# Kernel tuning notes

Hardware: AMD Instinct MI355X
Metric: run time of the kernel (lower is better)

## Reference

```python
import jax, jax.numpy as jnp
import numpy as np
from jax import lax

K = 3; PAD = 1; STR = 1; DIL = 1; DG = 16; MRM = 10.0


def _conv3(x, w, b):
    y = lax.conv_general_dilated(x, w, (1, 1), ((PAD, PAD), (PAD, PAD)),
                                 dimension_numbers=('NCHW', 'OIHW', 'NCHW'))
    return y + b[None, :, None, None]


def _leaky(x):
    return jnp.where(x >= 0, x, 0.1 * x)


def _bilinear_gather(img, py, px):
    # img: [B, dg, cg, H, W]; py, px: [B, dg, KK, H, W] sampling coords
    B, dg, cg, H, W = img.shape
    KK = py.shape[2]
    y0f = jnp.floor(py); x0f = jnp.floor(px)
    wy = py - y0f; wx = px - x0f          # bilinear fractions (grad flows via py/px)
    y0 = y0f.astype(jnp.int32); x0 = x0f.astype(jnp.int32)
    y1 = y0 + 1; x1 = x0 + 1
    imgf = img.reshape(B * dg, cg, H * W)

    def gather(yi, xi):
        valid = ((yi >= 0) & (yi < H) & (xi >= 0) & (xi < W)).astype(img.dtype)
        idx = jnp.clip(yi, 0, H - 1) * W + jnp.clip(xi, 0, W - 1)
        idxf = idx.reshape(B * dg, KK * H * W)
        v = jax.vmap(lambda im, ix: im[:, ix])(imgf, idxf)  # [B*dg, cg, KK*H*W]
        v = v.reshape(B, dg, cg, KK, H, W)
        return v * valid[:, :, None]  # zero padding outside image

    w00 = ((1 - wy) * (1 - wx))[:, :, None]
    w01 = ((1 - wy) * wx)[:, :, None]
    w10 = (wy * (1 - wx))[:, :, None]
    w11 = (wy * wx)[:, :, None]
    return (gather(y0, x0) * w00 + gather(y0, x1) * w01 +
            gather(y1, x0) * w10 + gather(y1, x1) * w11)


def reference(x, extra_feat, flow, w1, b1, w2, b2, w3, b3, weight):
    B, C, H, W = x.shape
    KK = K * K
    cg = C // DG
    P = DG * KK
    # offset/mask generating convnet
    h = _leaky(_conv3(extra_feat, w1, b1))
    h = _leaky(_conv3(h, w2, b2))
    o = _conv3(h, w3, b3)                       # [B, 3*P, H, W]
    o1, o2, m = jnp.split(o, 3, axis=1)
    off = MRM * jnp.tanh(jnp.concatenate([o1, o2], axis=1))  # [B, 2P, H, W]
    flow_yx = flow[:, ::-1]                      # flip(1): (x,y)->(y,x)
    off = off + jnp.tile(flow_yx, (1, P, 1, 1))
    off = off.reshape(B, DG, KK, 2, H, W)        # pair p=(g,k): channel 2p=y, 2p+1=x
    off_y = off[:, :, :, 0]
    off_x = off[:, :, :, 1]
    mask = jax.nn.sigmoid(m).reshape(B, DG, KK, H, W)

    ki = jnp.arange(KK)
    ky = (ki // K).astype(x.dtype) * DIL - PAD   # kernel row offsets
    kx = (ki % K).astype(x.dtype) * DIL - PAD
    base_h = jnp.arange(H, dtype=x.dtype) * STR
    base_w = jnp.arange(W, dtype=x.dtype) * STR
    py = base_h[None, None, None, :, None] + ky[None, None, :, None, None] + off_y
    px = base_w[None, None, None, None, :] + kx[None, None, :, None, None] + off_x

    img = x.reshape(B, DG, cg, H, W)
    val = _bilinear_gather(img, py, px) * mask[:, :, None]  # [B,dg,cg,KK,H,W]
    wk = weight.reshape(weight.shape[0], DG, cg, KK)
    # modulated deformable conv accumulate (bias=None in original forward)
    return jnp.einsum('bgckhw,ogck->bohw', val, wk)


def setup_inputs() -> dict:
    key = jax.random.key(0)
    ks = jax.random.split(key, 10)
    B, C, H, W = 2, 64, 128, 128
    OFFC = 3 * K * K * DG  # 432
    return {
        'x': jax.random.normal(ks[0], (B, C, H, W), jnp.float32),
        'extra_feat': jax.random.normal(ks[1], (B, 2 * C, H, W), jnp.float32),
        'flow': jax.random.normal(ks[2], (B, 2, H, W), jnp.float32),
        'w1': jax.random.normal(ks[3], (C, 2 * C, 3, 3), jnp.float32) * 0.05,
        'b1': jnp.zeros((C,), jnp.float32),
        'w2': jax.random.normal(ks[4], (C, C, 3, 3), jnp.float32) * 0.05,
        'b2': jnp.zeros((C,), jnp.float32),
        'w3': jax.random.normal(ks[5], (OFFC, C, 3, 3), jnp.float32) * 0.01,
        'b3': jnp.zeros((OFFC,), jnp.float32),
        'weight': jax.random.normal(ks[6], (C, C, 3, 3), jnp.float32) * 0.05,
    }
```

## Files before the change

### kernel.cpp

```cpp
#include <hip/hip_runtime.h>
#include <math.h>

constexpr int B_   = 2;
constexpr int C_   = 64;
constexpr int H_   = 128;
constexpr int W_   = 128;
constexpr int HW_  = H_ * W_;
constexpr int DG_  = 16;
constexpr int KK_  = 9;
constexpr int CG_  = 4;
constexpr int OFFC_ = 3 * KK_ * DG_;
constexpr int R_   = C_ * KK_;
constexpr int WP_  = 130;
constexpr int HWP_ = WP_ * WP_;

typedef _Float16 half8 __attribute__((ext_vector_type(8)));
typedef _Float16 half4 __attribute__((ext_vector_type(4)));
typedef float floatx4 __attribute__((ext_vector_type(4)));

__device__ __forceinline__ void gl_lds16(const _Float16* g, _Float16* l)
{
    __builtin_amdgcn_global_load_lds(
        (const __attribute__((address_space(1))) void*)g,
        (__attribute__((address_space(3))) void*)l, 16, 0, 0);
}

__device__ __forceinline__ int afrag_src(int c)
{
    const int cmf = c >> 6, cq = (c >> 4) & 3, cl = c & 15;
    return (cmf * 16 + cl) * 32 + cq * 8;
}

constexpr int SR0 = 288, SR1 = 432, SR2 = 1404, SR3 = 1548;
constexpr int SR4 = 1676, SR5 = 1804, SR6 = 1837;

__global__ __launch_bounds__(256) void setup_k(
    const float* __restrict__ x,  const float* __restrict__ ef,
    const float* __restrict__ w1, const float* __restrict__ w2,
    const float* __restrict__ w3, const float* __restrict__ wk,
    _Float16* __restrict__ w1A, _Float16* __restrict__ w2A,
    _Float16* __restrict__ w3A, _Float16* __restrict__ wkA,
    _Float16* __restrict__ ef_p, _Float16* __restrict__ xg,
    _Float16* __restrict__ h1p,  _Float16* __restrict__ h2p)
{
    const int bid = blockIdx.x;
    const int tid = threadIdx.x;

    if (bid < SR0) {
        constexpr int OC = 64, CH = 4;
        const int j = bid * 256 + tid;
        if (j >= 9 * CH * OC * 32) return;
        const int slab = j / (OC * 32);
        const int rem  = j - slab * (OC * 32);
        const int oc   = rem >> 5;
        const int jj   = rem & 31;
        const int t    = slab / CH;
        const int h    = slab - t * CH;
        const int ic   = h * 32 + jj;
        w1A[j] = (_Float16)w1[(size_t)oc * (128 * 9) + ic * 9 + t];
    } else if (bid < SR1) {
        constexpr int OC = 64, CH = 2;
        const int j = (bid - SR0) * 256 + tid;
        if (j >= 9 * CH * OC * 32) return;
        const int slab = j / (OC * 32);
        const int rem  = j - slab * (OC * 32);
        const int oc   = rem >> 5;
        const int jj   = rem & 31;
        const int t    = slab / CH;
        const int h    = slab - t * CH;
        const int ic   = h * 32 + jj;
        w2A[j] = (_Float16)w2[(size_t)oc * (64 * 9) + ic * 9 + t];
    } else if (bid < SR2) {
        constexpr int OC = OFFC_, CH = 2;
        const int j = (bid - SR1) * 256 + tid;
        if (j >= 9 * CH * OC * 32) return;
        const int slab = j / (OC * 32);
        const int rem  = j - slab * (OC * 32);
        const int oc   = rem >> 5;
        const int jj   = rem & 31;
        const int t    = slab / CH;
        const int h    = slab - t * CH;
        const int ic   = h * 32 + jj;
        w3A[j] = (_Float16)w3[(size_t)oc * (64 * 9) + ic * 9 + t];
    } else if (bid < SR3) {
        const int j = (bid - SR2) * 256 + tid;
        if (j >= 18 * 64 * 32) return;
        const int s   = j >> 11;
        const int rem = j & 2047;
        const int oc  = rem >> 5;
        const int jj  = rem & 31;
        const int k   = s >> 1;
        const int gc  = (s & 1) * 32 + jj;
        wkA[j] = (_Float16)wk[(size_t)oc * R_ + gc * 9 + k];
    } else if (bid < SR4) {
        const int lb  = bid - SR3;
        const int b   = lb >> 6;
        const int pix = (lb & 63) * 256 + tid;
        const int yp  = pix >> 7;
        const int xp  = pix & (W_ - 1);
        const float* ib = ef + (size_t)b * 128 * HW_ + pix;
#pragma unroll
        for (int c0 = 0; c0 < 128; c0 += 8) {
            half8 v;
#pragma unroll
            for (int j = 0; j < 8; ++j)
                v[j] = (_Float16)ib[(size_t)(c0 + j) * HW_];
            const int slab = c0 >> 5;
            *(half8*)&ef_p[((size_t)(slab * B_ + b) * HWP_
                            + (size_t)(yp + 1) * WP_ + (xp + 1)) * 32 + (c0 & 31)] = v;
        }
    } else if (bid < SR5) {
        const int lb  = bid - SR4;
        const int b   = lb >> 6;
        const int pix = (lb & 63) * 256 + tid;
        const float* ib = x + (size_t)b * C_ * HW_ + pix;
#pragma unroll
        for (int g = 0; g < DG_; ++g) {
            half4 v;
#pragma unroll
            for (int c = 0; c < 4; ++c)
                v[c] = (_Float16)ib[(size_t)(g * 4 + c) * HW_];
            *(half4*)&xg[((size_t)(b * DG_ + g) * HW_ + pix) * 4] = v;
        }
    } else {
        const int idx = (bid - SR5) * 256 + tid;
        if (idx >= 16 * 516) return;
        const int plane = idx / 516;
        const int p     = idx - plane * 516;
        int yp, xp;
        if (p < 130)      { yp = 0;            xp = p; }
        else if (p < 260) { yp = 129;          xp = p - 130; }
        else if (p < 388) { yp = 1 + (p - 260); xp = 0; }
        else              { yp = 1 + (p - 388); xp = 129; }
        _Float16* base;
        if (plane < 8)       base = ef_p + (size_t)plane * HWP_ * 32;
        else if (plane < 12) base = h1p + (size_t)(plane - 8) * HWP_ * 32;
        else                 base = h2p + (size_t)(plane - 12) * HWP_ * 32;
        _Float16* dst = base + ((size_t)yp * WP_ + xp) * 32;
        const half8 z = (half8){0, 0, 0, 0, 0, 0, 0, 0};
#pragma unroll
        for (int j = 0; j < 4; ++j)
            *(half8*)&dst[j * 8] = z;
    }
}

__global__ __launch_bounds__(256, 2) void conv1_mfma_k(
    const _Float16* __restrict__ inp, const _Float16* __restrict__ wA,
    const float* __restrict__ bias, _Float16* __restrict__ outp)
{
    __shared__ __align__(16) _Float16 Asm[18 * 2048];

    const int tid  = threadIdx.x;
    const int lane = tid & 63;
    const int wv   = tid >> 6;
    const int l15  = lane & 15;
    const int quad = lane >> 4;

    const int zx   = blockIdx.x;
    const int row  = zx >> 1;
    const int b    = row >> 7;
    const int y    = row & 127;
    const int px0  = (zx & 1) * 64 + wv * 16;

    const int sA = afrag_src(tid);

    const _Float16* bb[12];
#pragma unroll
    for (int h = 0; h < 4; ++h)
#pragma unroll
        for (int dy = 0; dy < 3; ++dy)
            bb[h * 3 + dy] = inp + ((size_t)(h * B_ + b) * HWP_
                                    + (size_t)(y + dy) * WP_ + px0 + l15) * 32 + quad * 8;

    floatx4 acc[4];
#pragma unroll
    for (int mf = 0; mf < 4; ++mf)
        acc[mf] = (floatx4){0.f, 0.f, 0.f, 0.f};

#pragma unroll
    for (int s = 0; s < 18; ++s)
        gl_lds16(wA + (size_t)s * 2048 + sA, Asm + s * 2048 + tid * 8);
    __syncthreads();

    const _Float16* abase = Asm + lane * 8;
#pragma unroll
    for (int ks = 0; ks < 18; ++ks) {
        const int t = ks >> 2, h = ks & 3;
        const int dy = t / 3, dx = t % 3;
        const half8 bfr = *(const half8*)&bb[h * 3 + dy][dx * 32];
#pragma unroll
        for (int mf = 0; mf < 4; ++mf) {
            const half8 afr = *(const half8*)&abase[ks * 2048 + mf * 512];
            acc[mf] = __builtin_amdgcn_mfma_f32_16x16x32_f16(afr, bfr, acc[mf], 0, 0, 0);
        }
    }
    __syncthreads();

#pragma unroll
    for (int s = 0; s < 18; ++s)
        gl_lds16(wA + (size_t)(18 + s) * 2048 + sA, Asm + s * 2048 + tid * 8);
    __syncthreads();

#pragma unroll
    for (int ks = 18; ks < 36; ++ks) {
        const int t = ks >> 2, h = ks & 3;
        const int dy = t / 3, dx = t % 3;
        const half8 bfr = *(const half8*)&bb[h * 3 + dy][dx * 32];
#pragma unroll
        for (int mf = 0; mf < 4; ++mf) {
            const half8 afr = *(const half8*)&abase[(ks - 18) * 2048 + mf * 512];
            acc[mf] = __builtin_amdgcn_mfma_f32_16x16x32_f16(afr, bfr, acc[mf], 0, 0, 0);
        }
    }

#pragma unroll
    for (int mf = 0; mf < 4; ++mf) {
        const int oc4 = mf * 16 + quad * 4;
        const float4 b4 = *(const float4*)&bias[oc4];
        half4 v4;
#pragma unroll
        for (int reg = 0; reg < 4; ++reg) {
            float r = acc[mf][reg] + ((const float*)&b4)[reg];
            r = (r >= 0.f) ? r : 0.1f * r;
            v4[reg] = (_Float16)r;
        }
        *(half4*)&outp[((size_t)((oc4 >> 5) * B_ + b) * HWP_
                        + (size_t)(y + 1) * WP_ + (px0 + l15 + 1)) * 32 + (oc4 & 31)] = v4;
    }
}

__global__ __launch_bounds__(256, 2) void conv2_mfma_k(
    const _Float16* __restrict__ inp, const _Float16* __restrict__ wA,
    const float* __restrict__ bias, _Float16* __restrict__ outp)
{
    __shared__ __align__(16) _Float16 Asm[18 * 2048];

    const int tid  = threadIdx.x;
    const int lane = tid & 63;
    const int wv   = tid >> 6;
    const int l15  = lane & 15;
    const int quad = lane >> 4;

    const int zx   = blockIdx.x;
    const int row  = zx >> 1;
    const int b    = row >> 7;
    const int y    = row & 127;
    const int px0  = (zx & 1) * 64 + wv * 16;

    const int sA = afrag_src(tid);

#pragma unroll
    for (int s = 0; s < 18; ++s)
        gl_lds16(wA + (size_t)s * 2048 + sA, Asm + s * 2048 + tid * 8);

    const _Float16* bb[6];
#pragma unroll
    for (int h = 0; h < 2; ++h)
#pragma unroll
        for (int dy = 0; dy < 3; ++dy)
            bb[h * 3 + dy] = inp + ((size_t)(h * B_ + b) * HWP_
                                    + (size_t)(y + dy) * WP_ + px0 + l15) * 32 + quad * 8;

    floatx4 acc[4];
#pragma unroll
    for (int mf = 0; mf < 4; ++mf)
        acc[mf] = (floatx4){0.f, 0.f, 0.f, 0.f};

    __syncthreads();

    const _Float16* abase = Asm + lane * 8;
#pragma unroll
    for (int ks = 0; ks < 18; ++ks) {
        const int t = ks >> 1, h = ks & 1;
        const int dy = t / 3, dx = t % 3;
        const half8 bfr = *(const half8*)&bb[h * 3 + dy][dx * 32];
#pragma unroll
        for (int mf = 0; mf < 4; ++mf) {
            const half8 afr = *(const half8*)&abase[ks * 2048 + mf * 512];
            acc[mf] = __builtin_amdgcn_mfma_f32_16x16x32_f16(afr, bfr, acc[mf], 0, 0, 0);
        }
    }

#pragma unroll
    for (int mf = 0; mf < 4; ++mf) {
        const int oc4 = mf * 16 + quad * 4;
        const float4 b4 = *(const float4*)&bias[oc4];
        half4 v4;
#pragma unroll
        for (int reg = 0; reg < 4; ++reg) {
            float r = acc[mf][reg] + ((const float*)&b4)[reg];
            r = (r >= 0.f) ? r : 0.1f * r;
            v4[reg] = (_Float16)r;
        }
        *(half4*)&outp[((size_t)((oc4 >> 5) * B_ + b) * HWP_
                        + (size_t)(y + 1) * WP_ + (px0 + l15 + 1)) * 32 + (oc4 & 31)] = v4;
    }
}

__global__ __launch_bounds__(256, 3) void conv3_mfma_k(
    const _Float16* __restrict__ h2p, const _Float16* __restrict__ w3A,
    const float* __restrict__ bias, const float* __restrict__ flow,
    _Float16* __restrict__ omh)
{
    __shared__ __align__(16) _Float16 Smem[17 * 1536];
    _Float16* Lds = Smem;

    const int tid  = threadIdx.x;
    const int lane = tid & 63;
    const int wv   = tid >> 6;
    const int l15  = lane & 15;
    const int quad = lane >> 4;

    const int row = blockIdx.x;
    const int b   = row >> 7;
    const int y   = row & 127;
    const int m0  = blockIdx.y * 48;
    const int px0 = wv * 32;

#pragma unroll
    for (int r = 0; r < 13; ++r) {
        const int c = r * 256 + tid;
        if (c < 17 * 192) {
            const int ks = c / 192;
            const int cl = c - ks * 192;
            const int cmf = cl >> 6, cq = (cl >> 4) & 3, ccl = cl & 15;
            gl_lds16(w3A + ((size_t)ks * OFFC_ + m0 + cmf * 16 + ccl) * 32 + cq * 8,
                     Smem + c * 8);
        }
    }

    half8 Af17[3];
#pragma unroll
    for (int mf = 0; mf < 3; ++mf)
        Af17[mf] = *(const half8*)&w3A[
            ((size_t)17 * OFFC_ + m0 + mf * 16 + l15) * 32 + quad * 8];

    const _Float16* bb[6];
#pragma unroll
    for (int h = 0; h < 2; ++h)
#pragma unroll
        for (int dy = 0; dy < 3; ++dy)
            bb[h * 3 + dy] = h2p + ((size_t)(h * B_ + b) * HWP_
                                    + (size_t)(y + dy) * WP_ + px0 + l15) * 32 + quad * 8;

    floatx4 acc[3][2];
#pragma unroll
    for (int mf = 0; mf < 3; ++mf)
#pragma unroll
        for (int nf = 0; nf < 2; ++nf)
            acc[mf][nf] = (floatx4){0.f, 0.f, 0.f, 0.f};

    __syncthreads();

    const _Float16* abase = Smem + lane * 8;
#pragma unroll
    for (int ks = 0; ks < 17; ++ks) {
        const int t = ks >> 1, h = ks & 1;
        const int dy = t / 3, dx = t % 3;
        const half8 b0 = *(const half8*)&bb[h * 3 + dy][dx * 32];
        const half8 b1 = *(const half8*)&bb[h * 3 + dy][(16 + dx) * 32];
#pragma unroll
        for (int mf = 0; mf < 3; ++mf) {
            const half8 afr = *(const half8*)&abase[ks * 1536 + mf * 512];
            acc[mf][0] = __builtin_amdgcn_mfma_f32_16x16x32_f16(afr, b0, acc[mf][0], 0, 0, 0);
            acc[mf][1] = __builtin_amdgcn_mfma_f32_16x16x32_f16(afr, b1, acc[mf][1], 0, 0, 0);
        }
    }
    {
        const half8 b0 = *(const half8*)&bb[5][2 * 32];
        const half8 b1 = *(const half8*)&bb[5][(16 + 2) * 32];
#pragma unroll
        for (int mf = 0; mf < 3; ++mf) {
            acc[mf][0] = __builtin_amdgcn_mfma_f32_16x16x32_f16(Af17[mf], b0, acc[mf][0], 0, 0, 0);
            acc[mf][1] = __builtin_amdgcn_mfma_f32_16x16x32_f16(Af17[mf], b1, acc[mf][1], 0, 0, 0);
        }
    }
    __syncthreads();

    const bool is_off = (blockIdx.y < 6);
    float flY[2], flX[2];
#pragma unroll
    for (int nf = 0; nf < 2; ++nf) {
        const int px = px0 + nf * 16 + l15;
        if (is_off) {
            flY[nf] = flow[(size_t)(b * 2 + 1) * HW_ + y * W_ + px];
            flX[nf] = flow[(size_t)(b * 2 + 0) * HW_ + y * W_ + px];
        }
    }
#pragma unroll
    for (int mf = 0; mf < 3; ++mf) {
        const float4 b4 = *(const float4*)&bias[m0 + mf * 16 + quad * 4];
#pragma unroll
        for (int nf = 0; nf < 2; ++nf) {
            const int px = px0 + nf * 16 + l15;
#pragma unroll
            for (int reg = 0; reg < 4; ++reg) {
                const int ocl = mf * 16 + quad * 4 + reg;
                float val = acc[mf][nf][reg] + ((const float*)&b4)[reg];
                if (is_off) {
                    const int slot = reg & 1;
                    const float fl = slot ? flX[nf] : flY[nf];
                    const float e = __expf(2.f * val);
                    val = 10.f * (1.f - __fdividef(2.f, e + 1.f)) + fl;
                } else {
                    val = __fdividef(1.f, 1.f + __expf(-val));
                }
                Lds[ocl * 132 + px] = (_Float16)val;
            }
        }
    }
    __syncthreads();

#pragma unroll
    for (int it = 0; it < 6; ++it) {
        const int j4 = it * 256 + tid;
        const int r  = j4 >> 5;
        const int c4 = j4 & 31;
        const int oc = m0 + r;
        int g, k, slot;
        if (oc < 2 * DG_ * KK_) {
            g = oc / 18;
            const int rem = oc - g * 18;
            k = rem >> 1;
            slot = rem & 1;
        } else {
            const int c = oc - 2 * DG_ * KK_;
            g = c / 9;
            k = c - g * 9;
            slot = 2;
        }
        const half4 hv = *(const half4*)&Lds[r * 132 + c4 * 4];
        *(half4*)&omh[((size_t)((b * DG_ * KK_ + g * KK_ + k) * 3 + slot)) * HW_
                      + y * W_ + c4 * 4] = hv;
    }
}

__global__ __launch_bounds__(256, 2) void gather_k(
    const _Float16* __restrict__ xg, const _Float16* __restrict__ omh,
    _Float16* __restrict__ valh)
{
    const int tid = threadIdx.x;
    const int pix = blockIdx.x * 256 + tid;
    const int zy  = blockIdx.y;
    const int b   = zy / KK_;
    const int k   = zy - b * KK_;
    const int yp  = pix >> 7;
    const int xp  = pix & (W_ - 1);
    const float fy = (float)(yp + (k / 3) - 1);
    const float fx = (float)(xp + (k % 3) - 1);

    float oyA[16], oxA[16], mA[16];
#pragma unroll
    for (int g = 0; g < DG_; ++g) {
        const size_t obase = ((size_t)((b * DG_ + g) * KK_ + k) * 3) * HW_ + pix;
        oyA[g] = (float)omh[obase];
        oxA[g] = (float)omh[obase + HW_];
        mA[g]  = (float)omh[obase + 2 * HW_];
    }

    half4 rec[16];
#pragma unroll
    for (int g = 0; g < DG_; ++g) {
        const float py = fy + oyA[g];
        const float px = fx + oxA[g];
        const float y0f = floorf(py);
        const float x0f = floorf(px);
        const float wy = py - y0f;
        const float wx = px - x0f;
        const int y0 = (int)y0f, x0 = (int)x0f;
        const int y1 = y0 + 1,  x1 = x0 + 1;
        const bool vy0 = ((unsigned)y0 < (unsigned)H_);
        const bool vy1 = ((unsigned)y1 < (unsigned)H_);
        const bool vx0 = ((unsigned)x0 < (unsigned)W_);
        const bool vx1 = ((unsigned)x1 < (unsigned)W_);
        const float w00 = vy0 && vx0 ? (1.f - wy) * (1.f - wx) : 0.f;
        const float w01 = vy0 && vx1 ? (1.f - wy) * wx         : 0.f;
        const float w10 = vy1 && vx0 ? wy * (1.f - wx)         : 0.f;
        const float w11 = vy1 && vx1 ? wy * wx                 : 0.f;
        const int i00 = (vy0 && vx0) ? y0 * W_ + x0 : 0;
        const int i01 = (vy0 && vx1) ? y0 * W_ + x1 : 0;
        const int i10 = (vy1 && vx0) ? y1 * W_ + x0 : 0;
        const int i11 = (vy1 && vx1) ? y1 * W_ + x1 : 0;

        const _Float16* xb = xg + (size_t)(b * DG_ + g) * HW_ * 4;
        const half4 p00 = *(const half4*)&xb[(size_t)i00 * 4];
        const half4 p01 = *(const half4*)&xb[(size_t)i01 * 4];
        const half4 p10 = *(const half4*)&xb[(size_t)i10 * 4];
        const half4 p11 = *(const half4*)&xb[(size_t)i11 * 4];

        half4 v4;
#pragma unroll
        for (int c = 0; c < CG_; ++c) {
            float v = w00 * (float)p00[c] + w01 * (float)p01[c]
                    + w10 * (float)p10[c] + w11 * (float)p11[c];
            v4[c] = (_Float16)(v * mA[g]);
        }
        rec[g] = v4;
    }

    _Float16* r0 = &valh[((size_t)((2 * k) * B_ + b) * HW_ + pix) * 32];
    _Float16* r1 = &valh[((size_t)((2 * k + 1) * B_ + b) * HW_ + pix) * 32];
#pragma unroll
    for (int j = 0; j < 4; ++j) {
        half8 w0, w1;
#pragma unroll
        for (int c = 0; c < 4; ++c) {
            w0[c]     = rec[2 * j][c];
            w0[c + 4] = rec[2 * j + 1][c];
            w1[c]     = rec[8 + 2 * j][c];
            w1[c + 4] = rec[9 + 2 * j][c];
        }
        *(half8*)&r0[j * 8] = w0;
        *(half8*)&r1[j * 8] = w1;
    }
}

__global__ __launch_bounds__(256, 2) void einsum_mfma_k(
    const _Float16* __restrict__ valh, const _Float16* __restrict__ wkA,
    float* __restrict__ out)
{
    __shared__ __align__(16) _Float16 Smem[18 * 2048];
    float* Lds = (float*)Smem;

    const int tid  = threadIdx.x;
    const int lane = tid & 63;
    const int wv   = tid >> 6;
    const int l15  = lane & 15;
    const int quad = lane >> 4;

    const int pixg0 = blockIdx.x * 64 + wv * 16;
    const int b     = pixg0 >> 14;
    const int pix0  = pixg0 & (HW_ - 1);

    const int sA = afrag_src(tid);

#pragma unroll
    for (int s = 0; s < 18; ++s)
        gl_lds16(wkA + (size_t)s * 2048 + sA, Smem + s * 2048 + tid * 8);

    floatx4 acc[4];
#pragma unroll
    for (int mf = 0; mf < 4; ++mf)
        acc[mf] = (floatx4){0.f, 0.f, 0.f, 0.f};

    half8 Bf[2];
    Bf[0] = *(const half8*)&valh[((size_t)(0 * B_ + b) * HW_ + pix0 + l15) * 32 + quad * 8];
    __syncthreads();

#pragma unroll
    for (int s = 0; s < 18; ++s) {
        const int cur = s & 1, nxt = cur ^ 1;
        if (s < 17) {
            const int s1 = s + 1;
            Bf[nxt] = *(const half8*)&valh[
                ((size_t)(s1 * B_ + b) * HW_ + pix0 + l15) * 32 + quad * 8];
        }
        const _Float16* abase = Smem + s * 2048 + lane * 8;
#pragma unroll
        for (int mf = 0; mf < 4; ++mf) {
            const half8 afr = *(const half8*)&abase[mf * 512];
            acc[mf] = __builtin_amdgcn_mfma_f32_16x16x32_f16(afr, Bf[cur], acc[mf], 0, 0, 0);
        }
    }
    __syncthreads();

    const int pxl = wv * 16 + l15;
#pragma unroll
    for (int mf = 0; mf < 4; ++mf)
#pragma unroll
        for (int reg = 0; reg < 4; ++reg)
            Lds[(mf * 16 + quad * 4 + reg) * 68 + pxl] = acc[mf][reg];
    __syncthreads();

    const int pixb = blockIdx.x * 64 & (HW_ - 1);
#pragma unroll
    for (int it = 0; it < 4; ++it) {
        const int j4 = it * 256 + tid;
        const int r  = j4 >> 4;
        const int c4 = j4 & 15;
        float4 v;
        v.x = Lds[r * 68 + c4 * 4 + 0];
        v.y = Lds[r * 68 + c4 * 4 + 1];
        v.z = Lds[r * 68 + c4 * 4 + 2];
        v.w = Lds[r * 68 + c4 * 4 + 3];
        *(float4*)&out[((size_t)(b * C_ + r)) * HW_ + pixb + c4 * 4] = v;
    }
}

extern "C" void kernel_launch(void* const* d_in, const int* in_sizes, int n_in,
                              void* d_out, int out_size, void* d_ws, size_t ws_size,
                              hipStream_t stream)
{
    const float* x    = (const float*)d_in[0];
    const float* ef   = (const float*)d_in[1];
    const float* flow = (const float*)d_in[2];
    const float* w1   = (const float*)d_in[3];
    const float* b1   = (const float*)d_in[4];
    const float* w2   = (const float*)d_in[5];
    const float* b2   = (const float*)d_in[6];
    const float* w3   = (const float*)d_in[7];
    const float* b3   = (const float*)d_in[8];
    const float* wk   = (const float*)d_in[9];
    float* out = (float*)d_out;

    _Float16* omh  = (_Float16*)d_ws;
    _Float16* valh = omh + (size_t)B_ * OFFC_ * HW_;
    _Float16* ef_p = valh + (size_t)18 * B_ * HW_ * 32;
    _Float16* xg   = ef_p + (size_t)4 * B_ * HWP_ * 32;
    _Float16* h1p  = xg + (size_t)B_ * HW_ * 64;
    _Float16* h2p  = h1p + (size_t)2 * B_ * HWP_ * 32;
    _Float16* w1A  = h2p + (size_t)2 * B_ * HWP_ * 32;
    _Float16* w2A  = w1A + 64 * 128 * 9;
    _Float16* w3A  = w2A + 64 * 64 * 9;
    _Float16* wkA  = w3A + OFFC_ * 64 * 9;

    setup_k<<<dim3(SR6), 256, 0, stream>>>(
        x, ef, w1, w2, w3, wk, w1A, w2A, w3A, wkA, ef_p, xg, h1p, h2p);

    conv1_mfma_k<<<dim3(B_ * H_ * 2), 256, 0, stream>>>(ef_p, w1A, b1, h1p);
    conv2_mfma_k<<<dim3(B_ * H_ * 2), 256, 0, stream>>>(h1p, w2A, b2, h2p);
    conv3_mfma_k<<<dim3(B_ * H_, 9), 256, 0, stream>>>(h2p, w3A, b3, flow, omh);

    gather_k<<<dim3(HW_ / 256, B_ * KK_), 256, 0, stream>>>(xg, omh, valh);
    einsum_mfma_k<<<dim3(B_ * HW_ / 64), 256, 0, stream>>>(valh, wkA, out);
}
```

Before: 189.3 us.

## Process two output rows per block in conv3 to reuse staged weights

The third offset/mask convolution now computes two image rows per block instead of one, which halves the grid in x. Each weight fragment staged in LDS then feeds MFMAs for both rows, and the overlapping input rows are shared. This halves the per-block weight staging and the LDS fragment reads per MFMA. In exchange the accumulator register count doubles, occupancy is lowered to 2 blocks per CU, and fewer blocks are available for latency hiding.

```diff
diff --git a/kernel.cpp b/kernel.cpp
--- a/kernel.cpp
+++ b/kernel.cpp
@@ -297,7 +297,7 @@
     }
 }
 
-__global__ __launch_bounds__(256, 3) void conv3_mfma_k(
+__global__ __launch_bounds__(256, 2) void conv3_mfma_k(
     const _Float16* __restrict__ h2p, const _Float16* __restrict__ w3A,
     const float* __restrict__ bias, const float* __restrict__ flow,
     _Float16* __restrict__ omh)
@@ -311,11 +311,11 @@
     const int l15  = lane & 15;
     const int quad = lane >> 4;
 
-    const int row = blockIdx.x;
-    const int b   = row >> 7;
-    const int y   = row & 127;
-    const int m0  = blockIdx.y * 48;
-    const int px0 = wv * 32;
+    const int row0 = blockIdx.x * 2;
+    const int b    = row0 >> 7;
+    const int y0   = row0 & 127;
+    const int m0   = blockIdx.y * 48;
+    const int px0  = wv * 32;
 
 #pragma unroll
     for (int r = 0; r < 13; ++r) {
@@ -335,20 +335,22 @@
         Af17[mf] = *(const half8*)&w3A[
             ((size_t)17 * OFFC_ + m0 + mf * 16 + l15) * 32 + quad * 8];
 
-    const _Float16* bb[6];
+    const _Float16* bb2[8];
 #pragma unroll
     for (int h = 0; h < 2; ++h)
 #pragma unroll
-        for (int dy = 0; dy < 3; ++dy)
-            bb[h * 3 + dy] = h2p + ((size_t)(h * B_ + b) * HWP_
-                                    + (size_t)(y + dy) * WP_ + px0 + l15) * 32 + quad * 8;
-
-    floatx4 acc[3][2];
+        for (int dyy = 0; dyy < 4; ++dyy)
+            bb2[h * 4 + dyy] = h2p + ((size_t)(h * B_ + b) * HWP_
+                                      + (size_t)(y0 + dyy) * WP_ + px0 + l15) * 32 + quad * 8;
+
+    floatx4 acc[3][2][2];
 #pragma unroll
     for (int mf = 0; mf < 3; ++mf)
 #pragma unroll
         for (int nf = 0; nf < 2; ++nf)
-            acc[mf][nf] = (floatx4){0.f, 0.f, 0.f, 0.f};
+#pragma unroll
+            for (int rr = 0; rr < 2; ++rr)
+                acc[mf][nf][rr] = (floatx4){0.f, 0.f, 0.f, 0.f};
 
     __syncthreads();
 
@@ -357,82 +359,101 @@
     for (int ks = 0; ks < 17; ++ks) {
         const int t = ks >> 1, h = ks & 1;
         const int dy = t / 3, dx = t % 3;
-        const half8 b0 = *(const half8*)&bb[h * 3 + dy][dx * 32];
-        const half8 b1 = *(const half8*)&bb[h * 3 + dy][(16 + dx) * 32];
+        half8 bfr[2][2];
+#pragma unroll
+        for (int rr = 0; rr < 2; ++rr)
+#pragma unroll
+            for (int nf = 0; nf < 2; ++nf)
+                bfr[rr][nf] = *(const half8*)&bb2[h * 4 + dy + rr][(nf * 16 + dx) * 32];
 #pragma unroll
         for (int mf = 0; mf < 3; ++mf) {
             const half8 afr = *(const half8*)&abase[ks * 1536 + mf * 512];
-            acc[mf][0] = __builtin_amdgcn_mfma_f32_16x16x32_f16(afr, b0, acc[mf][0], 0, 0, 0);
-            acc[mf][1] = __builtin_amdgcn_mfma_f32_16x16x32_f16(afr, b1, acc[mf][1], 0, 0, 0);
+#pragma unroll
+            for (int rr = 0; rr < 2; ++rr) {
+                acc[mf][0][rr] = __builtin_amdgcn_mfma_f32_16x16x32_f16(afr, bfr[rr][0], acc[mf][0][rr], 0, 0, 0);
+                acc[mf][1][rr] = __builtin_amdgcn_mfma_f32_16x16x32_f16(afr, bfr[rr][1], acc[mf][1][rr], 0, 0, 0);
+            }
         }
     }
     {
-        const half8 b0 = *(const half8*)&bb[5][2 * 32];
-        const half8 b1 = *(const half8*)&bb[5][(16 + 2) * 32];
-#pragma unroll
-        for (int mf = 0; mf < 3; ++mf) {
-            acc[mf][0] = __builtin_amdgcn_mfma_f32_16x16x32_f16(Af17[mf], b0, acc[mf][0], 0, 0, 0);
-            acc[mf][1] = __builtin_amdgcn_mfma_f32_16x16x32_f16(Af17[mf], b1, acc[mf][1], 0, 0, 0);
-        }
+        half8 bfr[2][2];
+#pragma unroll
+        for (int rr = 0; rr < 2; ++rr)
+#pragma unroll
+            for (int nf = 0; nf < 2; ++nf)
+                bfr[rr][nf] = *(const half8*)&bb2[4 + 2 + rr][(nf * 16 + 2) * 32];
+#pragma unroll
+        for (int mf = 0; mf < 3; ++mf)
+#pragma unroll
+            for (int rr = 0; rr < 2; ++rr) {
+                acc[mf][0][rr] = __builtin_amdgcn_mfma_f32_16x16x32_f16(Af17[mf], bfr[rr][0], acc[mf][0][rr], 0, 0, 0);
+                acc[mf][1][rr] = __builtin_amdgcn_mfma_f32_16x16x32_f16(Af17[mf], bfr[rr][1], acc[mf][1][rr], 0, 0, 0);
+            }
     }
     __syncthreads();
 
     const bool is_off = (blockIdx.y < 6);
-    float flY[2], flX[2];
-#pragma unroll
-    for (int nf = 0; nf < 2; ++nf) {
-        const int px = px0 + nf * 16 + l15;
-        if (is_off) {
-            flY[nf] = flow[(size_t)(b * 2 + 1) * HW_ + y * W_ + px];
-            flX[nf] = flow[(size_t)(b * 2 + 0) * HW_ + y * W_ + px];
-        }
-    }
+    float flY[2][2], flX[2][2];
+#pragma unroll
+    for (int rr = 0; rr < 2; ++rr)
+#pragma unroll
+        for (int nf = 0; nf < 2; ++nf) {
+            const int px = px0 + nf * 16 + l15;
+            if (is_off) {
+                flY[rr][nf] = flow[(size_t)(b * 2 + 1) * HW_ + (y0 + rr) * W_ + px];
+                flX[rr][nf] = flow[(size_t)(b * 2 + 0) * HW_ + (y0 + rr) * W_ + px];
+            }
+        }
 #pragma unroll
     for (int mf = 0; mf < 3; ++mf) {
         const float4 b4 = *(const float4*)&bias[m0 + mf * 16 + quad * 4];
 #pragma unroll
-        for (int nf = 0; nf < 2; ++nf) {
-            const int px = px0 + nf * 16 + l15;
-#pragma unroll
-            for (int reg = 0; reg < 4; ++reg) {
-                const int ocl = mf * 16 + quad * 4 + reg;
-                float val = acc[mf][nf][reg] + ((const float*)&b4)[reg];
-                if (is_off) {
-                    const int slot = reg & 1;
-                    const float fl = slot ? flX[nf] : flY[nf];
-                    const float e = __expf(2.f * val);
-                    val = 10.f * (1.f - __fdividef(2.f, e + 1.f)) + fl;
-                } else {
-                    val = __fdividef(1.f, 1.f + __expf(-val));
+        for (int rr = 0; rr < 2; ++rr)
+#pragma unroll
+            for (int nf = 0; nf < 2; ++nf) {
+                const int px = px0 + nf * 16 + l15;
+#pragma unroll
+                for (int reg = 0; reg < 4; ++reg) {
+                    const int ocl = mf * 16 + quad * 4 + reg;
+                    float val = acc[mf][nf][rr][reg] + ((const float*)&b4)[reg];
+                    if (is_off) {
+                        const int slot = reg & 1;
+                        const float fl = slot ? flX[rr][nf] : flY[rr][nf];
+                        const float e = __expf(2.f * val);
+                        val = 10.f * (1.f - __fdividef(2.f, e + 1.f)) + fl;
+                    } else {
+                        val = __fdividef(1.f, 1.f + __expf(-val));
+                    }
+                    Lds[rr * 6336 + ocl * 132 + px] = (_Float16)val;
                 }
-                Lds[ocl * 132 + px] = (_Float16)val;
             }
-        }
-    }
-    __syncthreads();
-
-#pragma unroll
-    for (int it = 0; it < 6; ++it) {
-        const int j4 = it * 256 + tid;
-        const int r  = j4 >> 5;
-        const int c4 = j4 & 31;
-        const int oc = m0 + r;
-        int g, k, slot;
-        if (oc < 2 * DG_ * KK_) {
-            g = oc / 18;
-            const int rem = oc - g * 18;
-            k = rem >> 1;
-            slot = rem & 1;
-        } else {
-            const int c = oc - 2 * DG_ * KK_;
-            g = c / 9;
-            k = c - g * 9;
-            slot = 2;
-        }
-        const half4 hv = *(const half4*)&Lds[r * 132 + c4 * 4];
-        *(half4*)&omh[((size_t)((b * DG_ * KK_ + g * KK_ + k) * 3 + slot)) * HW_
-                      + y * W_ + c4 * 4] = hv;
-    }
+    }
+    __syncthreads();
+
+#pragma unroll
+    for (int rr = 0; rr < 2; ++rr)
+#pragma unroll
+        for (int it = 0; it < 6; ++it) {
+            const int j4 = it * 256 + tid;
+            const int r  = j4 >> 5;
+            const int c4 = j4 & 31;
+            const int oc = m0 + r;
+            int g, k, slot;
+            if (oc < 2 * DG_ * KK_) {
+                g = oc / 18;
+                const int rem = oc - g * 18;
+                k = rem >> 1;
+                slot = rem & 1;
+            } else {
+                const int c = oc - 2 * DG_ * KK_;
+                g = c / 9;
+                k = c - g * 9;
+                slot = 2;
+            }
+            const half4 hv = *(const half4*)&Lds[rr * 6336 + r * 132 + c4 * 4];
+            *(half4*)&omh[((size_t)((b * DG_ * KK_ + g * KK_ + k) * 3 + slot)) * HW_
+                          + (y0 + rr) * W_ + c4 * 4] = hv;
+        }
 }
 
 __global__ __launch_bounds__(256, 2) void gather_k(
@@ -619,7 +640,7 @@
 
     conv1_mfma_k<<<dim3(B_ * H_ * 2), 256, 0, stream>>>(ef_p, w1A, b1, h1p);
     conv2_mfma_k<<<dim3(B_ * H_ * 2), 256, 0, stream>>>(h1p, w2A, b2, h2p);
-    conv3_mfma_k<<<dim3(B_ * H_, 9), 256, 0, stream>>>(h2p, w3A, b3, flow, omh);
+    conv3_mfma_k<<<dim3(B_ * H_ / 2, 9), 256, 0, stream>>>(h2p, w3A, b3, flow, omh);
 
     gather_k<<<dim3(HW_ / 256, B_ * KK_), 256, 0, stream>>>(xg, omh, valh);
     einsum_mfma_k<<<dim3(B_ * HW_ / 64), 256, 0, stream>>>(valh, wkA, out);
```

After: 182.1 us. -3.8%, faster.
